# Kernel tuning notes

Hardware: AMD Instinct MI355X
Metric: run time of the kernel (lower is better)

Reference implementation:

```python
import jax, jax.numpy as jnp
import numpy as np

B, N_ROWS, N_COLS, CTRL = 16384, 2048, 128, 1024
EPS = 1e-16


def setup_inputs() -> dict:
    key = jax.random.key(0)
    k1, k2, k3 = jax.random.split(key, 3)
    x = jax.random.normal(k1, (B, CTRL), dtype=jnp.float32)
    W_fc = jax.random.normal(k2, (CTRL, N_COLS + 6), dtype=jnp.float32) * 0.02
    b_fc = jnp.zeros((N_COLS + 6,), dtype=jnp.float32)
    M = jax.random.normal(k3, (N_ROWS, N_COLS), dtype=jnp.float32)
    # initial weighting: softmax of bias with w_bias[0]=100 -> ~one-hot at row 0
    w_bias = jnp.zeros((N_ROWS,), dtype=jnp.float32).at[0].set(100.0)
    w_prev = jnp.broadcast_to(jax.nn.softmax(w_bias), (B, N_ROWS))
    return {"x": x, "W_fc": W_fc, "b_fc": b_fc, "M": M, "w_prev": w_prev}


def reference(x, W_fc, b_fc, M, w_prev):
    # dense projection + split
    h = x @ W_fc + b_fc                      # [B, N_COLS+6]
    k = h[:, :N_COLS]                        # [B, N_COLS]
    beta = jax.nn.softplus(h[:, N_COLS:N_COLS + 1])          # [B, 1]
    g = jax.nn.sigmoid(h[:, N_COLS + 1:N_COLS + 2])          # [B, 1]
    s = jax.nn.softmax(h[:, N_COLS + 2:N_COLS + 5], axis=-1) # [B, 3]
    gamma = 1.0 + jax.nn.softplus(h[:, N_COLS + 5:N_COLS + 6])  # [B, 1]

    # content addressing: cosine similarity against every memory row
    k_norm = jnp.linalg.norm(k, axis=-1, keepdims=True)       # [B, 1]
    M_norm = jnp.linalg.norm(M, axis=-1)                      # [N_ROWS]
    sim = (k @ M.T) / (k_norm * M_norm[None, :] + EPS)        # [B, N_ROWS]
    w_c = jax.nn.softmax(beta * sim, axis=-1)

    # interpolation gate
    w_g = g * w_c + (1.0 - g) * w_prev

    # circular shift convolution (shifts -1, 0, +1)
    w_tilde = (s[:, 0:1] * jnp.roll(w_g, 1, axis=1)
               + s[:, 1:2] * w_g
               + s[:, 2:3] * jnp.roll(w_g, -1, axis=1))

    # sharpening
    w_pow = (w_tilde + EPS) ** gamma
    w = w_pow / jnp.sum(w_pow, axis=-1, keepdims=True)

    # weighted read
    r = w @ M                                                 # [B, N_COLS]
    return r
```

## Files before the change

### kernel.cpp

```cpp
#include <hip/hip_runtime.h>
#include <hip/hip_bf16.h>

#define NB    16384
#define NR    2048
#define NC    128
#define KCTRL 1024
#define EPSF  1e-16f
#define ESTR  2056
#define XSTR  1032

typedef __attribute__((ext_vector_type(8))) short bf16x8;
typedef __attribute__((ext_vector_type(4))) float f32x4;

__device__ __forceinline__ float softplus_f(float x) {
    return fmaxf(x, 0.f) + log1pf(__expf(-fabsf(x)));
}
__device__ __forceinline__ unsigned short f2bf(float f) {
    __hip_bfloat16 h = __float2bfloat16(f);
    return *(unsigned short*)&h;
}
__device__ __forceinline__ float bf2f(unsigned short u) {
    __hip_bfloat16 h;
    *(unsigned short*)&h = u;
    return __bfloat162float(h);
}

__device__ __forceinline__ size_t swz(int n, int k, int nch) {
    return ((size_t)((n >> 4) * nch + (k >> 5)) * 64 + ((k >> 3) & 3) * 16 + (n & 15)) * 8 + (k & 7);
}

__global__ __launch_bounds__(64) void prep_all(const float* __restrict__ M,
                                               unsigned short* __restrict__ Mb_sw,
                                               unsigned short* __restrict__ Mt_sw,
                                               float* __restrict__ imn,
                                               const float* __restrict__ W,
                                               unsigned short* __restrict__ Wt_sw) {
    const int bid = blockIdx.x;
    const int l = threadIdx.x;
    if (bid < NR) {
        const int i = bid;
        const float v0 = M[(size_t)i * NC + l];
        const float v1 = M[(size_t)i * NC + 64 + l];
        Mb_sw[swz(i, l, 4)]      = f2bf(v0);
        Mb_sw[swz(i, 64 + l, 4)] = f2bf(v1);
        Mt_sw[swz(l, i, 64)]      = f2bf(v0);
        Mt_sw[swz(64 + l, i, 64)] = f2bf(v1);
        float s = v0 * v0 + v1 * v1;
        #pragma unroll
        for (int m = 1; m < 64; m <<= 1) s += __shfl_xor(s, m);
        if (l == 0) imn[i] = 1.f / sqrtf(s);
    } else {
        const int k = bid - NR;
        Wt_sw[swz(l, k, 32)]      = f2bf(W[(size_t)k * 134 + l]);
        Wt_sw[swz(64 + l, k, 32)] = f2bf(W[(size_t)k * 134 + 64 + l]);
        if (l < 6) {
            Wt_sw[swz(128 + l, k, 32)] = f2bf(W[(size_t)k * 134 + 128 + l]);
        }
    }
}

__global__ __launch_bounds__(512, 4) void fused_ntm(const float* __restrict__ x,
                                                    const unsigned short* __restrict__ Wt_sw,
                                                    const float* __restrict__ bfc,
                                                    const unsigned short* __restrict__ Mb_sw,
                                                    const unsigned short* __restrict__ Mt_sw,
                                                    const float* __restrict__ imn,
                                                    const float* __restrict__ wprev,
                                                    float* __restrict__ out) {
    __shared__ __align__(16) unsigned short E_s[16][ESTR];
    __shared__ __align__(16) unsigned short k_s[16][136];
    __shared__ float h6s[16][6];
    __shared__ float ksum[16];
    __shared__ float scal_s[16][6];
    __shared__ float wred[16][8];
    __shared__ float fa_s[16], fc_s[16], invZ_s[16];

    unsigned short (*x_s)[XSTR] = (unsigned short(*)[XSTR])E_s;

    const int tid  = threadIdx.x;
    const int w    = tid >> 6;
    const int lane = tid & 63;
    const int quad = lane >> 4;
    const int l16  = lane & 15;
    const int b0   = blockIdx.x * 16;

    if (tid < 16) ksum[tid] = 0.f;
    #pragma unroll
    for (int p = 0; p < 8; p++) {
        const int idx = p * 512 + tid;
        const int row = idx >> 8;
        const int c4  = idx & 255;
        const float4 v = *(const float4*)(x + (size_t)(b0 + row) * KCTRL + c4 * 4);
        unsigned short* d = &x_s[row][c4 * 4];
        d[0] = f2bf(v.x); d[1] = f2bf(v.y); d[2] = f2bf(v.z); d[3] = f2bf(v.w);
    }
    __syncthreads();

    {
        f32x4 accF = {0.f, 0.f, 0.f, 0.f};
        f32x4 accH = {0.f, 0.f, 0.f, 0.f};
        const unsigned short* wbp = Wt_sw + (size_t)w * 32 * 512 + lane * 8;
        const unsigned short* whp = Wt_sw + (size_t)8 * 32 * 512 + lane * 8;
        #pragma unroll 4
        for (int i = 0; i < 32; i++) {
            const bf16x8 a = *(const bf16x8*)&x_s[l16][i * 32 + quad * 8];
            const bf16x8 b = *(const bf16x8*)(wbp + (size_t)i * 512);
            accF = __builtin_amdgcn_mfma_f32_16x16x32_bf16(a, b, accF, 0, 0, 0);
            if (w == 0) {
                const bf16x8 bh = *(const bf16x8*)(whp + (size_t)i * 512);
                accH = __builtin_amdgcn_mfma_f32_16x16x32_bf16(a, bh, accH, 0, 0, 0);
            }
        }
        __syncthreads();

        const float bb = bfc[w * 16 + l16];
        float part[4];
        #pragma unroll
        for (int reg = 0; reg < 4; reg++) {
            const int m = quad * 4 + reg;
            const float v = accF[reg] + bb;
            k_s[m][w * 16 + l16] = f2bf(v);
            part[reg] = v * v;
        }
        #pragma unroll
        for (int s = 1; s < 16; s <<= 1) {
            #pragma unroll
            for (int reg = 0; reg < 4; reg++) part[reg] += __shfl_xor(part[reg], s);
        }
        if (l16 == 0) {
            #pragma unroll
            for (int reg = 0; reg < 4; reg++) atomicAdd(&ksum[quad * 4 + reg], part[reg]);
        }
        if (w == 0 && l16 < 6) {
            const float bh = bfc[128 + l16];
            #pragma unroll
            for (int reg = 0; reg < 4; reg++) h6s[quad * 4 + reg][l16] = accH[reg] + bh;
        }
    }
    __syncthreads();

    if (tid < 16) {
        const float kn = sqrtf(ksum[tid]);
        const float* h = h6s[tid];
        const float beta = softplus_f(h[0]);
        const float g = 1.f / (1.f + __expf(-h[1]));
        const float m3 = fmaxf(h[2], fmaxf(h[3], h[4]));
        const float e0 = __expf(h[2] - m3), e1 = __expf(h[3] - m3), e2 = __expf(h[4] - m3);
        const float inv = 1.f / (e0 + e1 + e2);
        scal_s[tid][0] = beta / kn;
        scal_s[tid][1] = g;
        scal_s[tid][2] = e0 * inv;
        scal_s[tid][3] = e1 * inv;
        scal_s[tid][4] = e2 * inv;
        scal_s[tid][5] = 1.f + softplus_f(h[5]);
    }
    __syncthreads();

    {
        float cbs[4];
        #pragma unroll
        for (int reg = 0; reg < 4; reg++) cbs[reg] = scal_s[quad * 4 + reg][0];

        const bf16x8 af0 = *(const bf16x8*)&k_s[l16][quad * 8];
        const bf16x8 af1 = *(const bf16x8*)&k_s[l16][32 + quad * 8];
        const bf16x8 af2 = *(const bf16x8*)&k_s[l16][64 + quad * 8];
        const bf16x8 af3 = *(const bf16x8*)&k_s[l16][96 + quad * 8];

        float Sp[4] = {0.f, 0.f, 0.f, 0.f};
        #pragma unroll 4
        for (int t = 0; t < 16; t++) {
            const int nt = w * 16 + t;
            const unsigned short* bp = Mb_sw + (size_t)nt * 2048 + lane * 8;
            f32x4 aA = {0.f, 0.f, 0.f, 0.f};
            f32x4 aB = {0.f, 0.f, 0.f, 0.f};
            aA = __builtin_amdgcn_mfma_f32_16x16x32_bf16(af0, *(const bf16x8*)(bp), aA, 0, 0, 0);
            aB = __builtin_amdgcn_mfma_f32_16x16x32_bf16(af2, *(const bf16x8*)(bp + 1024), aB, 0, 0, 0);
            aA = __builtin_amdgcn_mfma_f32_16x16x32_bf16(af1, *(const bf16x8*)(bp + 512), aA, 0, 0, 0);
            aB = __builtin_amdgcn_mfma_f32_16x16x32_bf16(af3, *(const bf16x8*)(bp + 1536), aB, 0, 0, 0);
            const int n0 = nt * 16;
            const float im = imn[n0 + l16];
            #pragma unroll
            for (int reg = 0; reg < 4; reg++) {
                const float e = __expf((aA[reg] + aB[reg]) * cbs[reg] * im);
                E_s[quad * 4 + reg][n0 + l16] = f2bf(e);
                Sp[reg] += e;
            }
        }
        #pragma unroll
        for (int s = 1; s < 16; s <<= 1) {
            #pragma unroll
            for (int reg = 0; reg < 4; reg++) Sp[reg] += __shfl_xor(Sp[reg], s);
        }
        if (l16 == 0) {
            #pragma unroll
            for (int reg = 0; reg < 4; reg++) wred[quad * 4 + reg][w] = Sp[reg];
        }
    }
    __syncthreads();
    if (tid < 16) {
        float S = 0.f;
        #pragma unroll
        for (int i = 0; i < 8; i++) S += wred[tid][i];
        const float g = scal_s[tid][1];
        fa_s[tid] = g / S;
        fc_s[tid] = 1.f - g;
    }
    __syncthreads();

    {
        const int row  = tid >> 5;
        const int g    = tid & 31;
        const int base = tid & 32;
        const float s0 = scal_s[row][2], s1 = scal_s[row][3], s2 = scal_s[row][4];
        const float gmm = scal_s[row][5];
        const float fa = fa_s[row], fcm = fc_s[row];
        const float* wp = wprev + (size_t)(b0 + row) * NR;

        float Zp = 0.f;
        float carry = 0.f, E0sav = 0.f;
        #pragma unroll
        for (int j = 0; j < 8; j++) {
            const int c0 = (g + 32 * j) * 8;
            const bf16x8 E8 = *(const bf16x8*)&E_s[row][c0];
            float ef[8];
            #pragma unroll
            for (int i = 0; i < 8; i++) ef[i] = bf2f((unsigned short)E8[i]);
            const float eLraw = bf2f(E_s[row][(c0 + NR - 1) & (NR - 1)]);
            const float eRraw = bf2f(E_s[row][(c0 + 8) & (NR - 1)]);
            if (j == 0) E0sav = __shfl(ef[0], base);
            const float eL = (g == 0 && j > 0) ? carry : eLraw;
            const float eR = (g == 31 && j == 7) ? E0sav : eRraw;
            carry = __shfl(ef[7], base + 31);

            const float4 wa = *(const float4*)(wp + c0);
            const float4 wb = *(const float4*)(wp + c0 + 4);
            const float wpL = wp[(c0 + NR - 1) & (NR - 1)];
            const float wpR = wp[(c0 + 8) & (NR - 1)];

            float wg[10];
            wg[0] = fmaf(fa, eL,    fcm * wpL);
            wg[1] = fmaf(fa, ef[0], fcm * wa.x);
            wg[2] = fmaf(fa, ef[1], fcm * wa.y);
            wg[3] = fmaf(fa, ef[2], fcm * wa.z);
            wg[4] = fmaf(fa, ef[3], fcm * wa.w);
            wg[5] = fmaf(fa, ef[4], fcm * wb.x);
            wg[6] = fmaf(fa, ef[5], fcm * wb.y);
            wg[7] = fmaf(fa, ef[6], fcm * wb.z);
            wg[8] = fmaf(fa, ef[7], fcm * wb.w);
            wg[9] = fmaf(fa, eR,    fcm * wpR);

            bf16x8 out8;
            #pragma unroll
            for (int i = 0; i < 8; i++) {
                const float wt = fmaf(s0, wg[i], fmaf(s1, wg[i + 1], s2 * wg[i + 2])) + EPSF;
                const float pw = __expf(gmm * __logf(wt));
                Zp += pw;
                out8[i] = (short)f2bf(pw);
            }
            *(bf16x8*)&E_s[row][c0] = out8;
        }
        #pragma unroll
        for (int s = 1; s < 32; s <<= 1) Zp += __shfl_xor(Zp, s);
        if (g == 0) invZ_s[row] = 1.f / Zp;
    }
    __syncthreads();

    {
        f32x4 acc0 = {0.f, 0.f, 0.f, 0.f};
        f32x4 acc1 = {0.f, 0.f, 0.f, 0.f};
        f32x4 acc2 = {0.f, 0.f, 0.f, 0.f};
        f32x4 acc3 = {0.f, 0.f, 0.f, 0.f};
        const unsigned short* bp = Mt_sw + (size_t)w * 32768 + lane * 8;
        for (int k0 = 0; k0 < NR; k0 += 128) {
            const int C = k0 >> 5;
            const bf16x8 a0 = *(const bf16x8*)&E_s[l16][k0 + quad * 8];
            const bf16x8 a1 = *(const bf16x8*)&E_s[l16][k0 + 32 + quad * 8];
            const bf16x8 a2 = *(const bf16x8*)&E_s[l16][k0 + 64 + quad * 8];
            const bf16x8 a3 = *(const bf16x8*)&E_s[l16][k0 + 96 + quad * 8];
            const bf16x8 b0v = *(const bf16x8*)(bp + (size_t)C * 512);
            const bf16x8 b1v = *(const bf16x8*)(bp + (size_t)(C + 1) * 512);
            const bf16x8 b2v = *(const bf16x8*)(bp + (size_t)(C + 2) * 512);
            const bf16x8 b3v = *(const bf16x8*)(bp + (size_t)(C + 3) * 512);
            acc0 = __builtin_amdgcn_mfma_f32_16x16x32_bf16(a0, b0v, acc0, 0, 0, 0);
            acc1 = __builtin_amdgcn_mfma_f32_16x16x32_bf16(a1, b1v, acc1, 0, 0, 0);
            acc2 = __builtin_amdgcn_mfma_f32_16x16x32_bf16(a2, b2v, acc2, 0, 0, 0);
            acc3 = __builtin_amdgcn_mfma_f32_16x16x32_bf16(a3, b3v, acc3, 0, 0, 0);
        }
        #pragma unroll
        for (int reg = 0; reg < 4; reg++) {
            const int m = quad * 4 + reg;
            const float v = (acc0[reg] + acc1[reg]) + (acc2[reg] + acc3[reg]);
            out[(size_t)(b0 + m) * NC + w * 16 + l16] = v * invZ_s[m];
        }
    }
}

extern "C" void kernel_launch(void* const* d_in, const int* in_sizes, int n_in,
                              void* d_out, int out_size, void* d_ws, size_t ws_size,
                              hipStream_t stream) {
    const float* x     = (const float*)d_in[0];
    const float* Wfc   = (const float*)d_in[1];
    const float* bfc   = (const float*)d_in[2];
    const float* M     = (const float*)d_in[3];
    const float* wprev = (const float*)d_in[4];
    float* out = (float*)d_out;

    char* ws = (char*)d_ws;
    float*          imn   = (float*)(ws);
    unsigned short* Mb_sw = (unsigned short*)(ws + 8192);
    unsigned short* Mt_sw = (unsigned short*)(ws + 532480);
    unsigned short* Wt_sw = (unsigned short*)(ws + 1056768);

    hipLaunchKernelGGL(prep_all, dim3(NR + KCTRL), dim3(64), 0, stream,
                       M, Mb_sw, Mt_sw, imn, Wfc, Wt_sw);
    hipLaunchKernelGGL(fused_ntm, dim3(NB / 16), dim3(512), 0, stream,
                       x, Wt_sw, bfc, Mb_sw, Mt_sw, imn, wprev, out);
}
```

Measured before the change: 307.1 us.

## Halve batch rows per block to 8 and prefetch operands in sharpening loop

The fused kernel now processes 8 batch rows per block with 256 threads instead of 16 rows with 512 threads. It still uses 16x16 MFMAs, so the A operand duplicates rows and only half the outputs are kept, and each warp covers twice the columns or tiles. This halves LDS per block and doubles the grid, aiming for more resident blocks per CU and better latency hiding. The cost is wasted MFMA work and twice the reads of M and W per batch row. The shift/sharpen loop is also software-pipelined, loading the next chunk's E and w_prev values before computing the current one.

```diff
diff --git a/kernel.cpp b/kernel.cpp
--- a/kernel.cpp
+++ b/kernel.cpp
@@ -6,6 +6,7 @@
 #define NC    128
 #define KCTRL 1024
 #define EPSF  1e-16f
+#define NROW  8
 #define ESTR  2056
 #define XSTR  1032
 
@@ -59,7 +60,7 @@
     }
 }
 
-__global__ __launch_bounds__(512, 4) void fused_ntm(const float* __restrict__ x,
+__global__ __launch_bounds__(256, 4) void fused_ntm(const float* __restrict__ x,
                                                     const unsigned short* __restrict__ Wt_sw,
                                                     const float* __restrict__ bfc,
                                                     const unsigned short* __restrict__ Mb_sw,
@@ -67,13 +68,13 @@
                                                     const float* __restrict__ imn,
                                                     const float* __restrict__ wprev,
                                                     float* __restrict__ out) {
-    __shared__ __align__(16) unsigned short E_s[16][ESTR];
-    __shared__ __align__(16) unsigned short k_s[16][136];
-    __shared__ float h6s[16][6];
-    __shared__ float ksum[16];
-    __shared__ float scal_s[16][6];
-    __shared__ float wred[16][8];
-    __shared__ float fa_s[16], fc_s[16], invZ_s[16];
+    __shared__ __align__(16) unsigned short E_s[NROW][ESTR];
+    __shared__ __align__(16) unsigned short k_s[NROW][136];
+    __shared__ float h6s[NROW][6];
+    __shared__ float ksum[NROW];
+    __shared__ float scal_s[NROW][6];
+    __shared__ float wred[NROW][4];
+    __shared__ float fa_s[NROW], fc_s[NROW], invZ_s[NROW];
 
     unsigned short (*x_s)[XSTR] = (unsigned short(*)[XSTR])E_s;
 
@@ -82,12 +83,14 @@
     const int lane = tid & 63;
     const int quad = lane >> 4;
     const int l16  = lane & 15;
-    const int b0   = blockIdx.x * 16;
-
-    if (tid < 16) ksum[tid] = 0.f;
+    const int l8   = l16 & 7;
+    const int b0   = blockIdx.x * NROW;
+
+    if (tid < NROW) ksum[tid] = 0.f;
+
     #pragma unroll
     for (int p = 0; p < 8; p++) {
-        const int idx = p * 512 + tid;
+        const int idx = p * 256 + tid;
         const int row = idx >> 8;
         const int c4  = idx & 255;
         const float4 v = *(const float4*)(x + (size_t)(b0 + row) * KCTRL + c4 * 4);
@@ -97,49 +100,53 @@
     __syncthreads();
 
     {
-        f32x4 accF = {0.f, 0.f, 0.f, 0.f};
+        f32x4 acc0 = {0.f, 0.f, 0.f, 0.f};
+        f32x4 acc1 = {0.f, 0.f, 0.f, 0.f};
         f32x4 accH = {0.f, 0.f, 0.f, 0.f};
-        const unsigned short* wbp = Wt_sw + (size_t)w * 32 * 512 + lane * 8;
-        const unsigned short* whp = Wt_sw + (size_t)8 * 32 * 512 + lane * 8;
+        const unsigned short* p0 = Wt_sw + (size_t)w * 16384 + lane * 8;
+        const unsigned short* p1 = Wt_sw + (size_t)(w + 4) * 16384 + lane * 8;
+        const unsigned short* p2 = Wt_sw + (size_t)8 * 16384 + lane * 8;
         #pragma unroll 4
         for (int i = 0; i < 32; i++) {
-            const bf16x8 a = *(const bf16x8*)&x_s[l16][i * 32 + quad * 8];
-            const bf16x8 b = *(const bf16x8*)(wbp + (size_t)i * 512);
-            accF = __builtin_amdgcn_mfma_f32_16x16x32_bf16(a, b, accF, 0, 0, 0);
-            if (w == 0) {
-                const bf16x8 bh = *(const bf16x8*)(whp + (size_t)i * 512);
-                accH = __builtin_amdgcn_mfma_f32_16x16x32_bf16(a, bh, accH, 0, 0, 0);
-            }
-        }
-        __syncthreads();
-
-        const float bb = bfc[w * 16 + l16];
-        float part[4];
-        #pragma unroll
-        for (int reg = 0; reg < 4; reg++) {
-            const int m = quad * 4 + reg;
-            const float v = accF[reg] + bb;
-            k_s[m][w * 16 + l16] = f2bf(v);
-            part[reg] = v * v;
-        }
-        #pragma unroll
-        for (int s = 1; s < 16; s <<= 1) {
-            #pragma unroll
-            for (int reg = 0; reg < 4; reg++) part[reg] += __shfl_xor(part[reg], s);
-        }
-        if (l16 == 0) {
-            #pragma unroll
-            for (int reg = 0; reg < 4; reg++) atomicAdd(&ksum[quad * 4 + reg], part[reg]);
-        }
-        if (w == 0 && l16 < 6) {
-            const float bh = bfc[128 + l16];
-            #pragma unroll
-            for (int reg = 0; reg < 4; reg++) h6s[quad * 4 + reg][l16] = accH[reg] + bh;
-        }
-    }
-    __syncthreads();
-
-    if (tid < 16) {
+            const bf16x8 a = *(const bf16x8*)&x_s[l8][i * 32 + quad * 8];
+            acc0 = __builtin_amdgcn_mfma_f32_16x16x32_bf16(a, *(const bf16x8*)(p0 + (size_t)i * 512), acc0, 0, 0, 0);
+            acc1 = __builtin_amdgcn_mfma_f32_16x16x32_bf16(a, *(const bf16x8*)(p1 + (size_t)i * 512), acc1, 0, 0, 0);
+            if (w == 3) {
+                accH = __builtin_amdgcn_mfma_f32_16x16x32_bf16(a, *(const bf16x8*)(p2 + (size_t)i * 512), accH, 0, 0, 0);
+            }
+        }
+        if (quad < 2) {
+            const float bb0 = bfc[w * 16 + l16];
+            const float bb1 = bfc[(w + 4) * 16 + l16];
+            float part[4];
+            #pragma unroll
+            for (int reg = 0; reg < 4; reg++) {
+                const int m = quad * 4 + reg;
+                const float v0 = acc0[reg] + bb0;
+                const float v1 = acc1[reg] + bb1;
+                k_s[m][w * 16 + l16]       = f2bf(v0);
+                k_s[m][(w + 4) * 16 + l16] = f2bf(v1);
+                part[reg] = v0 * v0 + v1 * v1;
+            }
+            #pragma unroll
+            for (int s = 1; s < 16; s <<= 1) {
+                #pragma unroll
+                for (int reg = 0; reg < 4; reg++) part[reg] += __shfl_xor(part[reg], s);
+            }
+            if (l16 == 0) {
+                #pragma unroll
+                for (int reg = 0; reg < 4; reg++) atomicAdd(&ksum[quad * 4 + reg], part[reg]);
+            }
+            if (w == 3 && l16 < 6) {
+                const float bh = bfc[128 + l16];
+                #pragma unroll
+                for (int reg = 0; reg < 4; reg++) h6s[quad * 4 + reg][l16] = accH[reg] + bh;
+            }
+        }
+    }
+    __syncthreads();
+
+    if (tid < NROW) {
         const float kn = sqrtf(ksum[tid]);
         const float* h = h6s[tid];
         const float beta = softplus_f(h[0]);
@@ -159,17 +166,17 @@
     {
         float cbs[4];
         #pragma unroll
-        for (int reg = 0; reg < 4; reg++) cbs[reg] = scal_s[quad * 4 + reg][0];
-
-        const bf16x8 af0 = *(const bf16x8*)&k_s[l16][quad * 8];
-        const bf16x8 af1 = *(const bf16x8*)&k_s[l16][32 + quad * 8];
-        const bf16x8 af2 = *(const bf16x8*)&k_s[l16][64 + quad * 8];
-        const bf16x8 af3 = *(const bf16x8*)&k_s[l16][96 + quad * 8];
+        for (int reg = 0; reg < 4; reg++) cbs[reg] = scal_s[(quad & 1) * 4 + reg][0];
+
+        const bf16x8 af0 = *(const bf16x8*)&k_s[l8][quad * 8];
+        const bf16x8 af1 = *(const bf16x8*)&k_s[l8][32 + quad * 8];
+        const bf16x8 af2 = *(const bf16x8*)&k_s[l8][64 + quad * 8];
+        const bf16x8 af3 = *(const bf16x8*)&k_s[l8][96 + quad * 8];
 
         float Sp[4] = {0.f, 0.f, 0.f, 0.f};
         #pragma unroll 4
-        for (int t = 0; t < 16; t++) {
-            const int nt = w * 16 + t;
+        for (int t = 0; t < 32; t++) {
+            const int nt = w * 32 + t;
             const unsigned short* bp = Mb_sw + (size_t)nt * 2048 + lane * 8;
             f32x4 aA = {0.f, 0.f, 0.f, 0.f};
             f32x4 aB = {0.f, 0.f, 0.f, 0.f};
@@ -177,30 +184,32 @@
             aB = __builtin_amdgcn_mfma_f32_16x16x32_bf16(af2, *(const bf16x8*)(bp + 1024), aB, 0, 0, 0);
             aA = __builtin_amdgcn_mfma_f32_16x16x32_bf16(af1, *(const bf16x8*)(bp + 512), aA, 0, 0, 0);
             aB = __builtin_amdgcn_mfma_f32_16x16x32_bf16(af3, *(const bf16x8*)(bp + 1536), aB, 0, 0, 0);
-            const int n0 = nt * 16;
-            const float im = imn[n0 + l16];
-            #pragma unroll
-            for (int reg = 0; reg < 4; reg++) {
-                const float e = __expf((aA[reg] + aB[reg]) * cbs[reg] * im);
-                E_s[quad * 4 + reg][n0 + l16] = f2bf(e);
-                Sp[reg] += e;
-            }
-        }
-        #pragma unroll
-        for (int s = 1; s < 16; s <<= 1) {
-            #pragma unroll
-            for (int reg = 0; reg < 4; reg++) Sp[reg] += __shfl_xor(Sp[reg], s);
-        }
-        if (l16 == 0) {
-            #pragma unroll
-            for (int reg = 0; reg < 4; reg++) wred[quad * 4 + reg][w] = Sp[reg];
-        }
-    }
-    __syncthreads();
-    if (tid < 16) {
-        float S = 0.f;
-        #pragma unroll
-        for (int i = 0; i < 8; i++) S += wred[tid][i];
+            if (quad < 2) {
+                const int n0 = nt * 16;
+                const float im = imn[n0 + l16];
+                #pragma unroll
+                for (int reg = 0; reg < 4; reg++) {
+                    const float e = __expf((aA[reg] + aB[reg]) * cbs[reg] * im);
+                    E_s[quad * 4 + reg][n0 + l16] = f2bf(e);
+                    Sp[reg] += e;
+                }
+            }
+        }
+        if (quad < 2) {
+            #pragma unroll
+            for (int s = 1; s < 16; s <<= 1) {
+                #pragma unroll
+                for (int reg = 0; reg < 4; reg++) Sp[reg] += __shfl_xor(Sp[reg], s);
+            }
+            if (l16 == 0) {
+                #pragma unroll
+                for (int reg = 0; reg < 4; reg++) wred[quad * 4 + reg][w] = Sp[reg];
+            }
+        }
+    }
+    __syncthreads();
+    if (tid < NROW) {
+        const float S = wred[tid][0] + wred[tid][1] + wred[tid][2] + wred[tid][3];
         const float g = scal_s[tid][1];
         fa_s[tid] = g / S;
         fc_s[tid] = 1.f - g;
@@ -216,38 +225,49 @@
         const float fa = fa_s[row], fcm = fc_s[row];
         const float* wp = wprev + (size_t)(b0 + row) * NR;
 
-        float Zp = 0.f;
-        float carry = 0.f, E0sav = 0.f;
+        int c0 = g * 8;
+        bf16x8 E8c = *(const bf16x8*)&E_s[row][c0];
+        float eLc  = bf2f(E_s[row][(c0 + NR - 1) & (NR - 1)]);
+        float eRc  = bf2f(E_s[row][c0 + 8]);
+        float4 wac = *(const float4*)(wp + c0);
+        float4 wbc = *(const float4*)(wp + c0 + 4);
+        float wpLc = wp[(c0 + NR - 1) & (NR - 1)];
+        float wpRc = wp[c0 + 8];
+
+        float Zp = 0.f, carry = 0.f, E0sav = 0.f;
         #pragma unroll
         for (int j = 0; j < 8; j++) {
-            const int c0 = (g + 32 * j) * 8;
-            const bf16x8 E8 = *(const bf16x8*)&E_s[row][c0];
+            bf16x8 E8n; float eLn = 0.f, eRn = 0.f, wpLn = 0.f, wpRn = 0.f;
+            float4 wan, wbn;
+            if (j < 7) {
+                const int c1 = c0 + 256;
+                E8n  = *(const bf16x8*)&E_s[row][c1];
+                eLn  = bf2f(E_s[row][c1 - 1]);
+                eRn  = bf2f(E_s[row][(c1 + 8) & (NR - 1)]);
+                wan  = *(const float4*)(wp + c1);
+                wbn  = *(const float4*)(wp + c1 + 4);
+                wpLn = wp[c1 - 1];
+                wpRn = wp[(c1 + 8) & (NR - 1)];
+            }
             float ef[8];
             #pragma unroll
-            for (int i = 0; i < 8; i++) ef[i] = bf2f((unsigned short)E8[i]);
-            const float eLraw = bf2f(E_s[row][(c0 + NR - 1) & (NR - 1)]);
-            const float eRraw = bf2f(E_s[row][(c0 + 8) & (NR - 1)]);
+            for (int i = 0; i < 8; i++) ef[i] = bf2f((unsigned short)E8c[i]);
             if (j == 0) E0sav = __shfl(ef[0], base);
-            const float eL = (g == 0 && j > 0) ? carry : eLraw;
-            const float eR = (g == 31 && j == 7) ? E0sav : eRraw;
+            const float eL = (g == 0 && j > 0) ? carry : eLc;
+            const float eR = (g == 31 && j == 7) ? E0sav : eRc;
             carry = __shfl(ef[7], base + 31);
 
-            const float4 wa = *(const float4*)(wp + c0);
-            const float4 wb = *(const float4*)(wp + c0 + 4);
-            const float wpL = wp[(c0 + NR - 1) & (NR - 1)];
-            const float wpR = wp[(c0 + 8) & (NR - 1)];
-
             float wg[10];
-            wg[0] = fmaf(fa, eL,    fcm * wpL);
-            wg[1] = fmaf(fa, ef[0], fcm * wa.x);
-            wg[2] = fmaf(fa, ef[1], fcm * wa.y);
-            wg[3] = fmaf(fa, ef[2], fcm * wa.z);
-            wg[4] = fmaf(fa, ef[3], fcm * wa.w);
-            wg[5] = fmaf(fa, ef[4], fcm * wb.x);
-            wg[6] = fmaf(fa, ef[5], fcm * wb.y);
-            wg[7] = fmaf(fa, ef[6], fcm * wb.z);
-            wg[8] = fmaf(fa, ef[7], fcm * wb.w);
-            wg[9] = fmaf(fa, eR,    fcm * wpR);
+            wg[0] = fmaf(fa, eL,    fcm * wpLc);
+            wg[1] = fmaf(fa, ef[0], fcm * wac.x);
+            wg[2] = fmaf(fa, ef[1], fcm * wac.y);
+            wg[3] = fmaf(fa, ef[2], fcm * wac.z);
+            wg[4] = fmaf(fa, ef[3], fcm * wac.w);
+            wg[5] = fmaf(fa, ef[4], fcm * wbc.x);
+            wg[6] = fmaf(fa, ef[5], fcm * wbc.y);
+            wg[7] = fmaf(fa, ef[6], fcm * wbc.z);
+            wg[8] = fmaf(fa, ef[7], fcm * wbc.w);
+            wg[9] = fmaf(fa, eR,    fcm * wpRc);
 
             bf16x8 out8;
             #pragma unroll
@@ -258,6 +278,10 @@
                 out8[i] = (short)f2bf(pw);
             }
             *(bf16x8*)&E_s[row][c0] = out8;
+
+            c0 += 256;
+            E8c = E8n; eLc = eLn; eRc = eRn;
+            wac = wan; wbc = wbn; wpLc = wpLn; wpRc = wpRn;
         }
         #pragma unroll
         for (int s = 1; s < 32; s <<= 1) Zp += __shfl_xor(Zp, s);
@@ -265,18 +289,20 @@
     }
     __syncthreads();
 
-    {
+    #pragma unroll
+    for (int cpass = 0; cpass < 2; cpass++) {
+        const int c = w + cpass * 4;
         f32x4 acc0 = {0.f, 0.f, 0.f, 0.f};
         f32x4 acc1 = {0.f, 0.f, 0.f, 0.f};
         f32x4 acc2 = {0.f, 0.f, 0.f, 0.f};
         f32x4 acc3 = {0.f, 0.f, 0.f, 0.f};
-        const unsigned short* bp = Mt_sw + (size_t)w * 32768 + lane * 8;
+        const unsigned short* bp = Mt_sw + (size_t)c * 32768 + lane * 8;
         for (int k0 = 0; k0 < NR; k0 += 128) {
             const int C = k0 >> 5;
-            const bf16x8 a0 = *(const bf16x8*)&E_s[l16][k0 + quad * 8];
-            const bf16x8 a1 = *(const bf16x8*)&E_s[l16][k0 + 32 + quad * 8];
-            const bf16x8 a2 = *(const bf16x8*)&E_s[l16][k0 + 64 + quad * 8];
-            const bf16x8 a3 = *(const bf16x8*)&E_s[l16][k0 + 96 + quad * 8];
+            const bf16x8 a0 = *(const bf16x8*)&E_s[l8][k0 + quad * 8];
+            const bf16x8 a1 = *(const bf16x8*)&E_s[l8][k0 + 32 + quad * 8];
+            const bf16x8 a2 = *(const bf16x8*)&E_s[l8][k0 + 64 + quad * 8];
+            const bf16x8 a3 = *(const bf16x8*)&E_s[l8][k0 + 96 + quad * 8];
             const bf16x8 b0v = *(const bf16x8*)(bp + (size_t)C * 512);
             const bf16x8 b1v = *(const bf16x8*)(bp + (size_t)(C + 1) * 512);
             const bf16x8 b2v = *(const bf16x8*)(bp + (size_t)(C + 2) * 512);
@@ -286,11 +312,13 @@
             acc2 = __builtin_amdgcn_mfma_f32_16x16x32_bf16(a2, b2v, acc2, 0, 0, 0);
             acc3 = __builtin_amdgcn_mfma_f32_16x16x32_bf16(a3, b3v, acc3, 0, 0, 0);
         }
-        #pragma unroll
-        for (int reg = 0; reg < 4; reg++) {
-            const int m = quad * 4 + reg;
-            const float v = (acc0[reg] + acc1[reg]) + (acc2[reg] + acc3[reg]);
-            out[(size_t)(b0 + m) * NC + w * 16 + l16] = v * invZ_s[m];
+        if (quad < 2) {
+            #pragma unroll
+            for (int reg = 0; reg < 4; reg++) {
+                const int m = quad * 4 + reg;
+                const float v = (acc0[reg] + acc1[reg]) + (acc2[reg] + acc3[reg]);
+                out[(size_t)(b0 + m) * NC + c * 16 + l16] = v * invZ_s[m];
+            }
         }
     }
 }
@@ -313,6 +341,6 @@
 
     hipLaunchKernelGGL(prep_all, dim3(NR + KCTRL), dim3(64), 0, stream,
                        M, Mb_sw, Mt_sw, imn, Wfc, Wt_sw);
-    hipLaunchKernelGGL(fused_ntm, dim3(NB / 16), dim3(512), 0, stream,
+    hipLaunchKernelGGL(fused_ntm, dim3(NB / NROW), dim3(256), 0, stream,
                        x, Wt_sw, bfc, Mb_sw, Mt_sw, imn, wprev, out);
 }
```

Measured after the change: 352.2 us. 14.7% more time.
